# Kernel optimization log

Hardware: AMD Instinct MI355X
Metric: run time of the kernel (lower is better)

Reference implementation:

```python
import jax, jax.numpy as jnp
import numpy as np

DT = 0.02
TAU = 0.1


def setup_inputs() -> dict:
    key = jax.random.key(0)
    k_I, k_win, k_wrec, k_wout = jax.random.split(key, 4)
    M, N_in, T = 64, 2, 2000
    N, N_out = 512, 2
    I = jax.random.normal(k_I, (M, N_in, T), dtype=jnp.float32)
    x0 = jnp.zeros((1,), dtype=jnp.float32)
    W_in = jax.random.normal(k_win, (N, N_in), dtype=jnp.float32) / np.sqrt(N_in)
    # spectral-scale recurrent weights like a standard CTRNN init
    W_rec = jax.random.normal(k_wrec, (N, N), dtype=jnp.float32) * (1.5 / np.sqrt(N))
    b = jnp.zeros((N,), dtype=jnp.float32)
    # original inits W_out to zeros; use small random for a non-degenerate baseline
    W_out = jax.random.normal(k_wout, (N_out, N), dtype=jnp.float32) * 0.01
    return {"I": I, "x0": x0, "W_in": W_in, "W_rec": W_rec, "b": b, "W_out": W_out}


def reference(I, x0, W_in, W_rec, b, W_out):
    # I: (M, N_in, T); returns x, u: (M, N, T), y: (M, N_out, T)
    M, N_in, T = I.shape
    N = W_rec.shape[0]
    alpha = jnp.asarray(DT / TAU, dtype=I.dtype)
    x_init = jnp.full((M, N), x0[0], dtype=I.dtype)
    u_init = jnp.tanh(x_init)
    I_t = jnp.moveaxis(I, 2, 0)  # (T, M, N_in)

    def step(carry, It):
        x, u = carry
        # Euler step of tau*dx/dt = -x + W_rec u + W_in I + b
        x_new = x + alpha * (-x + u @ W_rec.T + It @ W_in.T + b)
        u_new = jnp.tanh(x_new)
        y_t = u_new @ W_out.T  # output uses u at t+1, as in the torch loop
        return (x_new, u_new), (x, u, y_t)

    _, (xs, us, ys) = jax.lax.scan(step, (x_init, u_init), I_t)
    # xs/us are the pre-step states (indices 0..T-1), matching x[:, :, :-1]
    x = jnp.moveaxis(xs, 0, 2)  # (M, N, T)
    u = jnp.moveaxis(us, 0, 2)  # (M, N, T)
    y = jnp.moveaxis(ys, 0, 2)  # (M, N_out, T)
    return (x, u, y)
```

## Files before the change

### kernel.cpp

```cpp
#include <hip/hip_runtime.h>

#define TT 2000
#define NN 512
#define MM 64
#define ALPHA 0.2f

typedef unsigned long long u64;

#define DPP_ROR_ADD(v, ctrl) do { \
  int _t = __builtin_amdgcn_update_dpp(0, __float_as_int(v), (ctrl), 0xF, 0xF, true); \
  (v) += __int_as_float(_t); } while (0)
#define ROW_REDUCE16(v) do { \
  DPP_ROR_ADD(v, 0x121); DPP_ROR_ADD(v, 0x122); \
  DPP_ROR_ADD(v, 0x124); DPP_ROR_ADD(v, 0x128); } while (0)

__device__ __forceinline__ float hsum4(float4 a){ return (a.x + a.y) + (a.z + a.w); }

__global__ __launch_bounds__(512, 2) void ctrnn(
    const float* __restrict__ I, const float* __restrict__ x0,
    const float* __restrict__ W_in, const float* __restrict__ W_rec,
    const float* __restrict__ b, const float* __restrict__ W_out,
    float* __restrict__ out_x, float* __restrict__ out_u, float* __restrict__ out_y,
    u64* __restrict__ pkt)
{
  __shared__ float u_lds[2][16 * 36];
  __shared__ float xbuf[2][128 * 9];
  __shared__ float ubuf[2][128 * 9];

  const int p = blockIdx.x >> 6, r = blockIdx.x & 63;
  const int tid = threadIdx.x;
  const int wave = tid >> 6, lane = tid & 63;
  const int g = tid >> 4, l16 = tid & 15;
  const int nb = p * 128 + g * 4;

  float4 w[4][8];
  #pragma unroll
  for (int rr = 0; rr < 4; rr++)
    #pragma unroll
    for (int jj = 0; jj < 8; jj++)
      w[rr][jj] = *(const float4*)(W_rec + (size_t)(nb + rr) * NN + jj * 64 + l16 * 4);

  const bool owner = (l16 == 0);
  float wi0[4], wi1[4], bb[4], xs[4], us[4];
  const float x00 = x0[0];
  const float u00 = tanhf(x00);
  #pragma unroll
  for (int j = 0; j < 4; j++){ xs[j] = x00; us[j] = u00; wi0[j] = wi1[j] = bb[j] = 0.f; }
  if (owner){
    #pragma unroll
    for (int j = 0; j < 4; j++){
      wi0[j] = W_in[2 * (nb + j)]; wi1[j] = W_in[2 * (nb + j) + 1]; bb[j] = b[nb + j];
    }
  }

  const bool yth = (p == 0) && (wave < 2) && (lane < 16);
  float4 wy[8];
  if (yth){
    #pragma unroll
    for (int c = 0; c < 8; c++)
      wy[c] = *(const float4*)(W_out + wave * NN + lane * 32 + 4 * c);
  }
  float yh0=0,yh1=0,yh2=0,yh3=0,yh4=0,yh5=0,yh6=0,yh7=0;

  u_lds[0][(tid >> 5) * 36 + (tid & 31)] = u00;
  __syncthreads();

  const float* Ib = I + (size_t)r * 2 * TT;
  float* ox = out_x + (size_t)r * NN * TT;
  float* ou = out_u + (size_t)r * NN * TT;
  float* oy = out_y + (size_t)r * 2 * TT;
  u64* pr = pkt + (size_t)r * NN;
  const int q  = tid - 128;
  const int rn = (q < p * 128) ? q : q + 128;

  for (int t = 0; t < TT; t++){
    const int cbuf = t & 1, nbuf = cbuf ^ 1;
    const int oct = (t >> 3) & 1, p8 = t & 7;

    float i0 = 0.f, i1 = 0.f;
    if (owner){ i0 = Ib[t]; i1 = Ib[TT + t]; }

    if (owner){
      #pragma unroll
      for (int j = 0; j < 4; j++){
        xbuf[oct][(g * 4 + j) * 9 + p8] = xs[j];
        ubuf[oct][(g * 4 + j) * 9 + p8] = us[j];
      }
    }

    if (yth){
      const float* ub = u_lds[cbuf] + lane * 36;
      float4 acc = make_float4(0,0,0,0);
      #pragma unroll
      for (int c = 0; c < 8; c++){
        float4 uv = *(const float4*)(ub + 4 * c);
        acc.x = fmaf(wy[c].x, uv.x, acc.x); acc.y = fmaf(wy[c].y, uv.y, acc.y);
        acc.z = fmaf(wy[c].z, uv.z, acc.z); acc.w = fmaf(wy[c].w, uv.w, acc.w);
      }
      float yv = hsum4(acc);
      ROW_REDUCE16(yv);
      yh0=yh1; yh1=yh2; yh2=yh3; yh3=yh4; yh4=yh5; yh5=yh6; yh6=yh7; yh7=yv;
      if (lane == 0 && p8 == 0 && t > 0){
        float* dst = oy + (size_t)wave * TT + (t - 8);
        *(float4*)dst       = make_float4(yh0, yh1, yh2, yh3);
        *(float4*)(dst + 4) = make_float4(yh4, yh5, yh6, yh7);
      }
    }

    float s[4];
    {
      const float* ub = u_lds[cbuf];
      float4 a0 = make_float4(0,0,0,0), a1 = a0, a2 = a0, a3 = a0;
      #pragma unroll
      for (int jj = 0; jj < 8; jj++){
        float4 uv = *(const float4*)(ub + (jj * 2 + (l16 >> 3)) * 36 + (l16 & 7) * 4);
        a0.x = fmaf(w[0][jj].x, uv.x, a0.x); a0.y = fmaf(w[0][jj].y, uv.y, a0.y);
        a0.z = fmaf(w[0][jj].z, uv.z, a0.z); a0.w = fmaf(w[0][jj].w, uv.w, a0.w);
        a1.x = fmaf(w[1][jj].x, uv.x, a1.x); a1.y = fmaf(w[1][jj].y, uv.y, a1.y);
        a1.z = fmaf(w[1][jj].z, uv.z, a1.z); a1.w = fmaf(w[1][jj].w, uv.w, a1.w);
        a2.x = fmaf(w[2][jj].x, uv.x, a2.x); a2.y = fmaf(w[2][jj].y, uv.y, a2.y);
        a2.z = fmaf(w[2][jj].z, uv.z, a2.z); a2.w = fmaf(w[2][jj].w, uv.w, a2.w);
        a3.x = fmaf(w[3][jj].x, uv.x, a3.x); a3.y = fmaf(w[3][jj].y, uv.y, a3.y);
        a3.z = fmaf(w[3][jj].z, uv.z, a3.z); a3.w = fmaf(w[3][jj].w, uv.w, a3.w);
      }
      s[0] = hsum4(a0); s[1] = hsum4(a1); s[2] = hsum4(a2); s[3] = hsum4(a3);
      ROW_REDUCE16(s[0]); ROW_REDUCE16(s[1]); ROW_REDUCE16(s[2]); ROW_REDUCE16(s[3]);
    }

    if (owner){
      #pragma unroll
      for (int j = 0; j < 4; j++){
        float pre = s[j] + fmaf(wi0[j], i0, fmaf(wi1[j], i1, bb[j]));
        xs[j] = fmaf(ALPHA, pre - xs[j], xs[j]);
        us[j] = tanhf(xs[j]);
      }
      *(float4*)(u_lds[nbuf] + (nb >> 5) * 36 + (nb & 31)) =
          make_float4(us[0], us[1], us[2], us[3]);
      const u64 tagw = ((u64)(unsigned)(t + 1)) << 32;
      u64* pd = pr + (size_t)nbuf * (MM * NN) + nb;
      #pragma unroll
      for (int j = 0; j < 4; j++)
        __hip_atomic_store(pd + j, tagw | (u64)__float_as_uint(us[j]),
                           __ATOMIC_RELAXED, __HIP_MEMORY_SCOPE_AGENT);
    }
    asm volatile("" ::: "memory");

    if (q >= 0){
      u64* ps = pr + (size_t)nbuf * (MM * NN) + rn;
      u64 pk = __hip_atomic_load(ps, __ATOMIC_RELAXED, __HIP_MEMORY_SCOPE_AGENT);
      while ((unsigned)(pk >> 32) != (unsigned)(t + 1)){
        __builtin_amdgcn_s_sleep(1);
        pk = __hip_atomic_load(ps, __ATOMIC_RELAXED, __HIP_MEMORY_SCOPE_AGENT);
      }
      u_lds[nbuf][(rn >> 5) * 36 + (rn & 31)] = __uint_as_float((unsigned)pk);
    }

    if (p8 == 0 && t > 0){
      const int arr = tid >> 8, n2 = (tid >> 1) & 127, h = tid & 1;
      const float* src = (arr ? ubuf[oct ^ 1] : xbuf[oct ^ 1]) + n2 * 9 + 4 * h;
      float* dst = (arr ? ou : ox) + (size_t)(p * 128 + n2) * TT + (t - 8) + 4 * h;
      *(float4*)dst = make_float4(src[0], src[1], src[2], src[3]);
    }

    __syncthreads();
  }

  if (yth){
    const float* ub = u_lds[0] + lane * 36;
    float4 acc = make_float4(0,0,0,0);
    #pragma unroll
    for (int c = 0; c < 8; c++){
      float4 uv = *(const float4*)(ub + 4 * c);
      acc.x = fmaf(wy[c].x, uv.x, acc.x); acc.y = fmaf(wy[c].y, uv.y, acc.y);
      acc.z = fmaf(wy[c].z, uv.z, acc.z); acc.w = fmaf(wy[c].w, uv.w, acc.w);
    }
    float yv = hsum4(acc);
    ROW_REDUCE16(yv);
    yh0=yh1; yh1=yh2; yh2=yh3; yh3=yh4; yh4=yh5; yh5=yh6; yh6=yh7; yh7=yv;
    if (lane == 0){
      float* dst = oy + (size_t)wave * TT + (TT - 8);
      *(float4*)dst       = make_float4(yh0, yh1, yh2, yh3);
      *(float4*)(dst + 4) = make_float4(yh4, yh5, yh6, yh7);
    }
  }
  {
    const int arr = tid >> 8, n2 = (tid >> 1) & 127, h = tid & 1;
    const float* src = (arr ? ubuf[1] : xbuf[1]) + n2 * 9 + 4 * h;
    float* dst = (arr ? ou : ox) + (size_t)(p * 128 + n2) * TT + (TT - 8) + 4 * h;
    *(float4*)dst = make_float4(src[0], src[1], src[2], src[3]);
  }
}

extern "C" void kernel_launch(void* const* d_in, const int* in_sizes, int n_in,
                              void* d_out, int out_size, void* d_ws, size_t ws_size,
                              hipStream_t stream){
  const float* I     = (const float*)d_in[0];
  const float* x0    = (const float*)d_in[1];
  const float* W_in  = (const float*)d_in[2];
  const float* W_rec = (const float*)d_in[3];
  const float* b     = (const float*)d_in[4];
  const float* W_out = (const float*)d_in[5];

  float* out_x = (float*)d_out;
  float* out_u = out_x + (size_t)MM * NN * TT;
  float* out_y = out_u + (size_t)MM * NN * TT;
  u64*   pkt   = (u64*)d_ws;

  ctrnn<<<MM * 4, 512, 0, stream>>>(I, x0, W_in, W_rec, b, W_out,
                                    out_x, out_u, out_y, pkt);
}
```

Before: 5.684 ms.

## Move output projection out of recurrent loop into separate parallel kernel

```diff
diff --git a/kernel.cpp b/kernel.cpp
--- a/kernel.cpp
+++ b/kernel.cpp
@@ -19,9 +19,9 @@
 __global__ __launch_bounds__(512, 2) void ctrnn(
     const float* __restrict__ I, const float* __restrict__ x0,
     const float* __restrict__ W_in, const float* __restrict__ W_rec,
-    const float* __restrict__ b, const float* __restrict__ W_out,
-    float* __restrict__ out_x, float* __restrict__ out_u, float* __restrict__ out_y,
-    u64* __restrict__ pkt)
+    const float* __restrict__ b,
+    float* __restrict__ out_x, float* __restrict__ out_u,
+    u64* __restrict__ pkt, float* __restrict__ uT)
 {
   __shared__ float u_lds[2][16 * 36];
   __shared__ float xbuf[2][128 * 9];
@@ -29,7 +29,6 @@
 
   const int p = blockIdx.x >> 6, r = blockIdx.x & 63;
   const int tid = threadIdx.x;
-  const int wave = tid >> 6, lane = tid & 63;
   const int g = tid >> 4, l16 = tid & 15;
   const int nb = p * 128 + g * 4;
 
@@ -39,6 +38,12 @@
     #pragma unroll
     for (int jj = 0; jj < 8; jj++)
       w[rr][jj] = *(const float4*)(W_rec + (size_t)(nb + rr) * NN + jj * 64 + l16 * 4);
+  #pragma unroll
+  for (int rr = 0; rr < 4; rr++)
+    #pragma unroll
+    for (int jj = 0; jj < 8; jj++)
+      asm volatile("" : "+v"(w[rr][jj].x), "+v"(w[rr][jj].y),
+                        "+v"(w[rr][jj].z), "+v"(w[rr][jj].w));
 
   const bool owner = (l16 == 0);
   float wi0[4], wi1[4], bb[4], xs[4], us[4];
@@ -53,22 +58,12 @@
     }
   }
 
-  const bool yth = (p == 0) && (wave < 2) && (lane < 16);
-  float4 wy[8];
-  if (yth){
-    #pragma unroll
-    for (int c = 0; c < 8; c++)
-      wy[c] = *(const float4*)(W_out + wave * NN + lane * 32 + 4 * c);
-  }
-  float yh0=0,yh1=0,yh2=0,yh3=0,yh4=0,yh5=0,yh6=0,yh7=0;
-
   u_lds[0][(tid >> 5) * 36 + (tid & 31)] = u00;
   __syncthreads();
 
   const float* Ib = I + (size_t)r * 2 * TT;
   float* ox = out_x + (size_t)r * NN * TT;
   float* ou = out_u + (size_t)r * NN * TT;
-  float* oy = out_y + (size_t)r * 2 * TT;
   u64* pr = pkt + (size_t)r * NN;
   const int q  = tid - 128;
   const int rn = (q < p * 128) ? q : q + 128;
@@ -85,25 +80,6 @@
       for (int j = 0; j < 4; j++){
         xbuf[oct][(g * 4 + j) * 9 + p8] = xs[j];
         ubuf[oct][(g * 4 + j) * 9 + p8] = us[j];
-      }
-    }
-
-    if (yth){
-      const float* ub = u_lds[cbuf] + lane * 36;
-      float4 acc = make_float4(0,0,0,0);
-      #pragma unroll
-      for (int c = 0; c < 8; c++){
-        float4 uv = *(const float4*)(ub + 4 * c);
-        acc.x = fmaf(wy[c].x, uv.x, acc.x); acc.y = fmaf(wy[c].y, uv.y, acc.y);
-        acc.z = fmaf(wy[c].z, uv.z, acc.z); acc.w = fmaf(wy[c].w, uv.w, acc.w);
-      }
-      float yv = hsum4(acc);
-      ROW_REDUCE16(yv);
-      yh0=yh1; yh1=yh2; yh2=yh3; yh3=yh4; yh4=yh5; yh5=yh6; yh6=yh7; yh7=yv;
-      if (lane == 0 && p8 == 0 && t > 0){
-        float* dst = oy + (size_t)wave * TT + (t - 8);
-        *(float4*)dst       = make_float4(yh0, yh1, yh2, yh3);
-        *(float4*)(dst + 4) = make_float4(yh4, yh5, yh6, yh7);
       }
     }
 
@@ -165,30 +141,44 @@
     __syncthreads();
   }
 
-  if (yth){
-    const float* ub = u_lds[0] + lane * 36;
-    float4 acc = make_float4(0,0,0,0);
-    #pragma unroll
-    for (int c = 0; c < 8; c++){
-      float4 uv = *(const float4*)(ub + 4 * c);
-      acc.x = fmaf(wy[c].x, uv.x, acc.x); acc.y = fmaf(wy[c].y, uv.y, acc.y);
-      acc.z = fmaf(wy[c].z, uv.z, acc.z); acc.w = fmaf(wy[c].w, uv.w, acc.w);
-    }
-    float yv = hsum4(acc);
-    ROW_REDUCE16(yv);
-    yh0=yh1; yh1=yh2; yh2=yh3; yh3=yh4; yh4=yh5; yh5=yh6; yh6=yh7; yh7=yv;
-    if (lane == 0){
-      float* dst = oy + (size_t)wave * TT + (TT - 8);
-      *(float4*)dst       = make_float4(yh0, yh1, yh2, yh3);
-      *(float4*)(dst + 4) = make_float4(yh4, yh5, yh6, yh7);
-    }
-  }
   {
     const int arr = tid >> 8, n2 = (tid >> 1) & 127, h = tid & 1;
     const float* src = (arr ? ubuf[1] : xbuf[1]) + n2 * 9 + 4 * h;
     float* dst = (arr ? ou : ox) + (size_t)(p * 128 + n2) * TT + (TT - 8) + 4 * h;
     *(float4*)dst = make_float4(src[0], src[1], src[2], src[3]);
   }
+  if (owner)
+    *(float4*)(uT + (size_t)r * NN + nb) = make_float4(us[0], us[1], us[2], us[3]);
+}
+
+__global__ __launch_bounds__(256) void y_out(
+    const float* __restrict__ W_out, const float* __restrict__ ou,
+    const float* __restrict__ uT, float* __restrict__ oy)
+{
+  __shared__ float w0[NN], w1[NN];
+  const int m = blockIdx.x, tid = threadIdx.x;
+  for (int i = tid; i < NN; i += 256){ w0[i] = W_out[i]; w1[i] = W_out[NN + i]; }
+  __syncthreads();
+  const int t = blockIdx.y * 256 + tid;
+  if (t >= TT) return;
+  float acc0 = 0.f, acc1 = 0.f;
+  if (t + 1 < TT){
+    const float* um = ou + (size_t)m * NN * TT + (t + 1);
+    #pragma unroll 4
+    for (int n = 0; n < NN; n++){
+      float uv = um[(size_t)n * TT];
+      acc0 = fmaf(w0[n], uv, acc0); acc1 = fmaf(w1[n], uv, acc1);
+    }
+  } else {
+    const float* um = uT + (size_t)m * NN;
+    #pragma unroll 4
+    for (int n = 0; n < NN; n++){
+      float uv = um[n];
+      acc0 = fmaf(w0[n], uv, acc0); acc1 = fmaf(w1[n], uv, acc1);
+    }
+  }
+  oy[(size_t)m * 2 * TT + t]      = acc0;
+  oy[(size_t)m * 2 * TT + TT + t] = acc1;
 }
 
 extern "C" void kernel_launch(void* const* d_in, const int* in_sizes, int n_in,
@@ -205,7 +195,10 @@
   float* out_u = out_x + (size_t)MM * NN * TT;
   float* out_y = out_u + (size_t)MM * NN * TT;
   u64*   pkt   = (u64*)d_ws;
-
-  ctrnn<<<MM * 4, 512, 0, stream>>>(I, x0, W_in, W_rec, b, W_out,
-                                    out_x, out_u, out_y, pkt);
+  float* uT    = (float*)((char*)d_ws + (size_t)2 * MM * NN * sizeof(u64));
+
+  ctrnn<<<MM * 4, 512, 0, stream>>>(I, x0, W_in, W_rec, b,
+                                    out_x, out_u, pkt, uT);
+  dim3 gy(MM, (TT + 255) / 256);
+  y_out<<<gy, 256, 0, stream>>>(W_out, out_u, uT, out_y);
 }
```

Measured after the change: 5.893 ms. 3.7% more time.
